# Kernel optimization log

Hardware: AMD Instinct MI355X
Metric: run time of the kernel (lower is better)

The kernel has to match this reference:

```python
import jax, jax.numpy as jnp
import numpy as np


def setup_inputs() -> dict:
    key = jax.random.key(0)
    k1, k2, k3 = jax.random.split(key, 3)
    B, H, W = 32, 512, 512
    N = H * W  # tokens
    K = 32768  # positive_trials
    decision_scores = jax.random.normal(k1, (B, N, 2), dtype=jnp.float32)
    s_map = jax.random.uniform(k2, (B, 1, H, W), dtype=jnp.float32)
    # uniform noise for gumbel sampling, kept away from {0,1} for log stability
    u = jax.random.uniform(k3, (B, N, 2), dtype=jnp.float32, minval=1e-6, maxval=1.0 - 1e-6)
    return {"decision_scores": decision_scores, "s_map": s_map, "u": u, "positive_trials": K}


def reference(decision_scores, s_map, u, positive_trials):
    B, N, _ = decision_scores.shape
    # gumbel_softmax(hard=False, tau=1): softmax(logits + gumbel_noise)
    gumbel = -jnp.log(-jnp.log(u))
    logp = jax.nn.log_softmax(decision_scores + gumbel, axis=-1)  # [B, N, 2]
    # soft_decisions = p[..., 0]
    # Tokenizer: [B, 1, H, W] -> [B, N, 1]; use channel 0 as salience score.
    scores = s_map.reshape(B, 1, -1).transpose(0, 2, 1)[..., 0]  # [B, N]
    # argsort descending, take top-k indices == lax.top_k indices
    _, idx = jax.lax.top_k(scores, positive_trials)  # [B, K]
    trials = jnp.zeros((B, N), dtype=decision_scores.dtype)
    trials = trials.at[jnp.arange(B)[:, None], idx].set(1.0)  # scatter ones
    # BCE(sum): -sum(t*log(p) + (1-t)*log(1-p)); with 2-class softmax, 1-p0 = p1.
    # torch BCE clamps log terms at -100.
    logp0 = jnp.clip(logp[..., 0], -100.0)
    logp1 = jnp.clip(logp[..., 1], -100.0)
    loss = -jnp.sum(trials * logp0 + (1.0 - trials) * logp1)
    return loss
```

## Files before the change

### kernel.cpp

```cpp
#include <hip/hip_runtime.h>

#define NB    4096
#define CAP   1024
#define BATCH 32
#define NTOK  262144
#define PT    1024
#define LOSS_BLOCKS 4096

__device__ __forceinline__ int bucket_of(float v) {
    int b = (int)(v * (float)NB);
    return b > NB - 1 ? NB - 1 : b;
}

__global__ __launch_bounds__(PT) void prep_kernel(const float* __restrict__ smap,
                                                  const int* __restrict__ kptr,
                                                  float* __restrict__ T,
                                                  int* __restrict__ ncut) {
    __shared__ int   hist[NB];
    __shared__ int   sA[PT];
    __shared__ int   sB[PT];
    __shared__ float sv[CAP];
    __shared__ int   si[CAP];
    __shared__ int   cnt_s, tb_s, R_s;

    const int tid = threadIdx.x;
    const int b   = blockIdx.x;

    for (int i = tid; i < NB; i += PT) hist[i] = 0;
    if (tid == 0) cnt_s = 0;
    __syncthreads();

    const float4* src = (const float4*)(smap + (size_t)b * NTOK);
    const int NF4 = NTOK / 4;
    for (int i = tid; i < NF4; i += PT) {
        float4 v = src[i];
        atomicAdd(&hist[bucket_of(v.x)], 1);
        atomicAdd(&hist[bucket_of(v.y)], 1);
        atomicAdd(&hist[bucket_of(v.z)], 1);
        atomicAdd(&hist[bucket_of(v.w)], 1);
    }
    __syncthreads();

    const int C = NB / PT;
    int base = tid * C;
    int csum = hist[base] + hist[base + 1] + hist[base + 2] + hist[base + 3];
    sA[tid] = csum;
    __syncthreads();

    int* pin = sA; int* pout = sB;
    for (int st = 1; st < PT; st <<= 1) {
        int v = pin[tid] + ((tid + st < PT) ? pin[tid + st] : 0);
        pout[tid] = v;
        __syncthreads();
        int* t_ = pin; pin = pout; pout = t_;
    }
    int above = (tid < PT - 1) ? pin[tid + 1] : 0;

    const int K = *kptr;
    int cum = above;
    for (int i = C - 1; i >= 0; i--) {
        int hb = hist[base + i];
        if (cum < K && cum + hb >= K) { tb_s = base + i; R_s = K - cum; }
        cum += hb;
    }
    __syncthreads();
    const int tb = tb_s, R = R_s;

    for (int i = tid; i < NF4; i += PT) {
        float4 v = src[i];
        float vals[4] = {v.x, v.y, v.z, v.w};
#pragma unroll
        for (int c = 0; c < 4; c++) {
            if (bucket_of(vals[c]) == tb) {
                int p = atomicAdd(&cnt_s, 1);
                if (p < CAP) { sv[p] = vals[c]; si[p] = 4 * i + c; }
            }
        }
    }
    __syncthreads();

    int M = cnt_s;
    if (M > CAP || R > M || R < 1) {
        if (tid == 0) { T[b] = (float)tb / (float)NB; ncut[b] = 0x7fffffff; }
        return;
    }
    for (int i = tid; i < M; i += PT) {
        float vi = sv[i]; int ii = si[i];
        int r = 0;
        for (int j = 0; j < M; j++) {
            float vj = sv[j];
            r += (vj > vi) || (vj == vi && si[j] < ii);
        }
        if (r == R - 1) { T[b] = vi; ncut[b] = ii; }
    }
}

__device__ __forceinline__ float token_loss(float d0, float d1, float u0, float u1,
                                            bool sel) {
    float g0 = -__logf(-__logf(u0));
    float g1 = -__logf(-__logf(u1));
    float dd = (d0 + g0) - (d1 + g1);
    float l  = __logf(1.f + __expf(-fabsf(dd)));
    float lp0 = (dd >= 0.f) ? -l      : dd - l;
    float lp1 = (dd >= 0.f) ? -l - dd : -l;
    lp0 = fmaxf(lp0, -100.f); lp1 = fmaxf(lp1, -100.f);
    return sel ? -lp0 : -lp1;
}

__global__ void loss_kernel(const float* __restrict__ ds, const float* __restrict__ u,
                            const float* __restrict__ smap, const float* __restrict__ T,
                            const int* __restrict__ ncut, float* __restrict__ partials) {
    int tid = blockIdx.x * blockDim.x + threadIdx.x;
    int b  = tid >> 15;
    int p8 = tid & 32767;
    const float4* ds4 = (const float4*)(ds + (size_t)b * NTOK * 2);
    const float4* u4  = (const float4*)(u  + (size_t)b * NTOK * 2);
    const float4* s4  = (const float4*)(smap + (size_t)b * NTOK);

    float4 d0 = ds4[4 * p8 + 0];
    float4 d1 = ds4[4 * p8 + 1];
    float4 d2 = ds4[4 * p8 + 2];
    float4 d3 = ds4[4 * p8 + 3];
    float4 u0 = u4[4 * p8 + 0];
    float4 u1 = u4[4 * p8 + 1];
    float4 u2 = u4[4 * p8 + 2];
    float4 u3 = u4[4 * p8 + 3];
    float4 sa = s4[2 * p8 + 0];
    float4 sb = s4[2 * p8 + 1];

    float Tb = T[b];
    int   nc = ncut[b];
    int   n0 = p8 << 3;

    bool e0 = (sa.x > Tb) || (sa.x == Tb && (n0 + 0) <= nc);
    bool e1 = (sa.y > Tb) || (sa.y == Tb && (n0 + 1) <= nc);
    bool e2 = (sa.z > Tb) || (sa.z == Tb && (n0 + 2) <= nc);
    bool e3 = (sa.w > Tb) || (sa.w == Tb && (n0 + 3) <= nc);
    bool e4 = (sb.x > Tb) || (sb.x == Tb && (n0 + 4) <= nc);
    bool e5 = (sb.y > Tb) || (sb.y == Tb && (n0 + 5) <= nc);
    bool e6 = (sb.z > Tb) || (sb.z == Tb && (n0 + 6) <= nc);
    bool e7 = (sb.w > Tb) || (sb.w == Tb && (n0 + 7) <= nc);

    float acc = token_loss(d0.x, d0.y, u0.x, u0.y, e0)
              + token_loss(d0.z, d0.w, u0.z, u0.w, e1)
              + token_loss(d1.x, d1.y, u1.x, u1.y, e2)
              + token_loss(d1.z, d1.w, u1.z, u1.w, e3)
              + token_loss(d2.x, d2.y, u2.x, u2.y, e4)
              + token_loss(d2.z, d2.w, u2.z, u2.w, e5)
              + token_loss(d3.x, d3.y, u3.x, u3.y, e6)
              + token_loss(d3.z, d3.w, u3.z, u3.w, e7);

    for (int off = 32; off > 0; off >>= 1) acc += __shfl_down(acc, off, 64);
    __shared__ float red[4];
    int lane = threadIdx.x & 63, wv = threadIdx.x >> 6;
    if (lane == 0) red[wv] = acc;
    __syncthreads();
    if (threadIdx.x == 0)
        partials[blockIdx.x] = red[0] + red[1] + red[2] + red[3];
}

__global__ void reduce_kernel(const float* __restrict__ partials, float* __restrict__ out) {
    float acc = 0.f;
    for (int i = threadIdx.x; i < LOSS_BLOCKS; i += blockDim.x) acc += partials[i];
    for (int off = 32; off > 0; off >>= 1) acc += __shfl_down(acc, off, 64);
    __shared__ float red[16];
    int lane = threadIdx.x & 63, wv = threadIdx.x >> 6;
    if (lane == 0) red[wv] = acc;
    __syncthreads();
    if (threadIdx.x == 0) {
        float s = 0.f;
        for (int w = 0; w < (int)(blockDim.x >> 6); w++) s += red[w];
        out[0] = s;
    }
}

extern "C" void kernel_launch(void* const* d_in, const int* in_sizes, int n_in,
                              void* d_out, int out_size, void* d_ws, size_t ws_size,
                              hipStream_t stream) {
    const float* ds   = (const float*)d_in[0];
    const float* smap = (const float*)d_in[1];
    const float* u    = (const float*)d_in[2];
    const int*   kptr = (const int*)d_in[3];

    float* T    = (float*)d_ws;
    int*   ncut = (int*)(T + BATCH);
    float* partials = (float*)(ncut + BATCH);

    prep_kernel<<<BATCH, PT, 0, stream>>>(smap, kptr, T, ncut);
    loss_kernel<<<LOSS_BLOCKS, 256, 0, stream>>>(ds, u, smap, T, ncut, partials);
    reduce_kernel<<<1, 1024, 0, stream>>>(partials, (float*)d_out);
}
```

Before: 233.9 us.

## Split top-k threshold prep into multi-block histogram, select, collect and refine kernels

The single prep kernel ran only one block per batch (32 blocks) and streamed each batch's salience map twice. It is replaced by a 512-block histogram kernel writing partial histograms to global memory, a select kernel that merges them and finds the threshold bucket, a 256-block collect kernel that gathers candidates with global atomics, and a refine kernel that ranks them. The loss kernel also switches to nontemporal loads for the decision scores and noise. The aim is to spread the salience scan across many more CUs, at the cost of extra launches, global histogram traffic and global atomic contention.

```diff
diff --git a/kernel.cpp b/kernel.cpp
--- a/kernel.cpp
+++ b/kernel.cpp
@@ -4,87 +4,128 @@
 #define CAP   1024
 #define BATCH 32
 #define NTOK  262144
-#define PT    1024
+#define HB    512
+#define HPB   16
 #define LOSS_BLOCKS 4096
+
+typedef float floatx4 __attribute__((ext_vector_type(4)));
 
 __device__ __forceinline__ int bucket_of(float v) {
     int b = (int)(v * (float)NB);
     return b > NB - 1 ? NB - 1 : b;
 }
 
-__global__ __launch_bounds__(PT) void prep_kernel(const float* __restrict__ smap,
-                                                  const int* __restrict__ kptr,
-                                                  float* __restrict__ T,
-                                                  int* __restrict__ ncut) {
-    __shared__ int   hist[NB];
-    __shared__ int   sA[PT];
-    __shared__ int   sB[PT];
-    __shared__ float sv[CAP];
-    __shared__ int   si[CAP];
-    __shared__ int   cnt_s, tb_s, R_s;
-
+__global__ void hist_kernel(const float* __restrict__ smap, int* __restrict__ ghist) {
+    __shared__ int lh[NB];
+    for (int i = threadIdx.x; i < NB; i += 256) lh[i] = 0;
+    __syncthreads();
+    const int b  = blockIdx.x / HPB;
+    const int cb = blockIdx.x % HPB;
+    const int chunk = NTOK / HPB;
+    const float4* src = (const float4*)(smap + (size_t)b * NTOK + (size_t)cb * chunk);
+    for (int i = threadIdx.x; i < chunk / 4; i += 256) {
+        float4 v = src[i];
+        atomicAdd(&lh[bucket_of(v.x)], 1);
+        atomicAdd(&lh[bucket_of(v.y)], 1);
+        atomicAdd(&lh[bucket_of(v.z)], 1);
+        atomicAdd(&lh[bucket_of(v.w)], 1);
+    }
+    __syncthreads();
+    int* out = ghist + (size_t)blockIdx.x * NB;
+    for (int i = threadIdx.x; i < NB; i += 256) out[i] = lh[i];
+}
+
+__global__ __launch_bounds__(1024) void select_kernel(const int* __restrict__ ghist,
+                                                      const int* __restrict__ kptr,
+                                                      int* __restrict__ tbR,
+                                                      int* __restrict__ cnt) {
+    __shared__ int hist[NB];
+    __shared__ int sA[1024];
+    __shared__ int sB[1024];
     const int tid = threadIdx.x;
     const int b   = blockIdx.x;
-
-    for (int i = tid; i < NB; i += PT) hist[i] = 0;
-    if (tid == 0) cnt_s = 0;
-    __syncthreads();
-
-    const float4* src = (const float4*)(smap + (size_t)b * NTOK);
-    const int NF4 = NTOK / 4;
-    for (int i = tid; i < NF4; i += PT) {
-        float4 v = src[i];
-        atomicAdd(&hist[bucket_of(v.x)], 1);
-        atomicAdd(&hist[bucket_of(v.y)], 1);
-        atomicAdd(&hist[bucket_of(v.z)], 1);
-        atomicAdd(&hist[bucket_of(v.w)], 1);
-    }
-    __syncthreads();
-
-    const int C = NB / PT;
+    if (tid == 0) cnt[b] = 0;
+
+    const int C = NB / 1024;
     int base = tid * C;
+    const int* gh0 = ghist + (size_t)b * HPB * NB;
+#pragma unroll
+    for (int i = 0; i < C; i++) {
+        int s = 0;
+        for (int c = 0; c < HPB; c++) s += gh0[c * NB + base + i];
+        hist[base + i] = s;
+    }
     int csum = hist[base] + hist[base + 1] + hist[base + 2] + hist[base + 3];
     sA[tid] = csum;
     __syncthreads();
 
     int* pin = sA; int* pout = sB;
-    for (int st = 1; st < PT; st <<= 1) {
-        int v = pin[tid] + ((tid + st < PT) ? pin[tid + st] : 0);
+    for (int st = 1; st < 1024; st <<= 1) {
+        int v = pin[tid] + ((tid + st < 1024) ? pin[tid + st] : 0);
         pout[tid] = v;
         __syncthreads();
         int* t_ = pin; pin = pout; pout = t_;
     }
-    int above = (tid < PT - 1) ? pin[tid + 1] : 0;
+    int above = (tid < 1023) ? pin[tid + 1] : 0;
 
     const int K = *kptr;
     int cum = above;
     for (int i = C - 1; i >= 0; i--) {
         int hb = hist[base + i];
-        if (cum < K && cum + hb >= K) { tb_s = base + i; R_s = K - cum; }
+        if (cum < K && cum + hb >= K) {
+            tbR[2 * b]     = base + i;
+            tbR[2 * b + 1] = K - cum;
+        }
         cum += hb;
     }
-    __syncthreads();
-    const int tb = tb_s, R = R_s;
-
-    for (int i = tid; i < NF4; i += PT) {
+}
+
+__global__ void collect_kernel(const float* __restrict__ smap, const int* __restrict__ tbR,
+                               int* __restrict__ cnt, float* __restrict__ cval,
+                               int* __restrict__ cidx) {
+    const int cbpb = 8;
+    const int b  = blockIdx.x / cbpb;
+    const int cb = blockIdx.x % cbpb;
+    const int chunk = NTOK / cbpb;
+    const int tb = tbR[2 * b];
+    const float4* src = (const float4*)(smap + (size_t)b * NTOK + (size_t)cb * chunk);
+    const int base_n = cb * chunk;
+    for (int i = threadIdx.x; i < chunk / 4; i += 256) {
         float4 v = src[i];
         float vals[4] = {v.x, v.y, v.z, v.w};
 #pragma unroll
-        for (int c = 0; c < 4; c++) {
-            if (bucket_of(vals[c]) == tb) {
-                int p = atomicAdd(&cnt_s, 1);
-                if (p < CAP) { sv[p] = vals[c]; si[p] = 4 * i + c; }
+        for (int s = 0; s < 4; s++) {
+            if (bucket_of(vals[s]) == tb) {
+                int p = atomicAdd(&cnt[b], 1);
+                if (p < CAP) {
+                    cval[b * CAP + p] = vals[s];
+                    cidx[b * CAP + p] = base_n + 4 * i + s;
+                }
             }
         }
     }
-    __syncthreads();
-
-    int M = cnt_s;
-    if (M > CAP || R > M || R < 1) {
-        if (tid == 0) { T[b] = (float)tb / (float)NB; ncut[b] = 0x7fffffff; }
+}
+
+__global__ void refine_kernel(const int* __restrict__ tbR, const int* __restrict__ cnt,
+                              const float* __restrict__ cval, const int* __restrict__ cidx,
+                              float* __restrict__ T, int* __restrict__ ncut) {
+    const int b = blockIdx.x;
+    const int R = tbR[2 * b + 1];
+    int M = cnt[b];
+    bool ovf = (M > CAP);
+    if (M > CAP) M = CAP;
+    __shared__ float sv[CAP];
+    __shared__ int   si[CAP];
+    for (int i = threadIdx.x; i < M; i += 256) {
+        sv[i] = cval[b * CAP + i];
+        si[i] = cidx[b * CAP + i];
+    }
+    __syncthreads();
+    if (ovf || R > M || R < 1) {
+        if (threadIdx.x == 0) { T[b] = (float)tbR[2 * b] / (float)NB; ncut[b] = 0x7fffffff; }
         return;
     }
-    for (int i = tid; i < M; i += PT) {
+    for (int i = threadIdx.x; i < M; i += 256) {
         float vi = sv[i]; int ii = si[i];
         int r = 0;
         for (int j = 0; j < M; j++) {
@@ -113,18 +154,18 @@
     int tid = blockIdx.x * blockDim.x + threadIdx.x;
     int b  = tid >> 15;
     int p8 = tid & 32767;
-    const float4* ds4 = (const float4*)(ds + (size_t)b * NTOK * 2);
-    const float4* u4  = (const float4*)(u  + (size_t)b * NTOK * 2);
-    const float4* s4  = (const float4*)(smap + (size_t)b * NTOK);
-
-    float4 d0 = ds4[4 * p8 + 0];
-    float4 d1 = ds4[4 * p8 + 1];
-    float4 d2 = ds4[4 * p8 + 2];
-    float4 d3 = ds4[4 * p8 + 3];
-    float4 u0 = u4[4 * p8 + 0];
-    float4 u1 = u4[4 * p8 + 1];
-    float4 u2 = u4[4 * p8 + 2];
-    float4 u3 = u4[4 * p8 + 3];
+    const floatx4* ds4 = (const floatx4*)(ds + (size_t)b * NTOK * 2);
+    const floatx4* u4  = (const floatx4*)(u  + (size_t)b * NTOK * 2);
+    const float4*  s4  = (const float4*)(smap + (size_t)b * NTOK);
+
+    floatx4 d0 = __builtin_nontemporal_load(&ds4[4 * p8 + 0]);
+    floatx4 d1 = __builtin_nontemporal_load(&ds4[4 * p8 + 1]);
+    floatx4 d2 = __builtin_nontemporal_load(&ds4[4 * p8 + 2]);
+    floatx4 d3 = __builtin_nontemporal_load(&ds4[4 * p8 + 3]);
+    floatx4 u0 = __builtin_nontemporal_load(&u4[4 * p8 + 0]);
+    floatx4 u1 = __builtin_nontemporal_load(&u4[4 * p8 + 1]);
+    floatx4 u2 = __builtin_nontemporal_load(&u4[4 * p8 + 2]);
+    floatx4 u3 = __builtin_nontemporal_load(&u4[4 * p8 + 3]);
     float4 sa = s4[2 * p8 + 0];
     float4 sb = s4[2 * p8 + 1];
 
@@ -182,11 +223,19 @@
     const float* u    = (const float*)d_in[2];
     const int*   kptr = (const int*)d_in[3];
 
-    float* T    = (float*)d_ws;
-    int*   ncut = (int*)(T + BATCH);
-    float* partials = (float*)(ncut + BATCH);
-
-    prep_kernel<<<BATCH, PT, 0, stream>>>(smap, kptr, T, ncut);
+    int*   ghist = (int*)d_ws;
+    int*   cnt   = ghist + HB * NB;
+    int*   tbR   = cnt + BATCH;
+    float* T     = (float*)(tbR + 2 * BATCH);
+    int*   ncut  = (int*)(T + BATCH);
+    float* cval  = (float*)(ncut + BATCH);
+    int*   cidx  = (int*)(cval + BATCH * CAP);
+    float* partials = (float*)(cidx + BATCH * CAP);
+
+    hist_kernel<<<HB, 256, 0, stream>>>(smap, ghist);
+    select_kernel<<<BATCH, 1024, 0, stream>>>(ghist, kptr, tbR, cnt);
+    collect_kernel<<<256, 256, 0, stream>>>(smap, tbR, cnt, cval, cidx);
+    refine_kernel<<<BATCH, 256, 0, stream>>>(tbR, cnt, cval, cidx, T, ncut);
     loss_kernel<<<LOSS_BLOCKS, 256, 0, stream>>>(ds, u, smap, T, ncut, partials);
     reduce_kernel<<<1, 1024, 0, stream>>>(partials, (float*)d_out);
 }
```

After: 213.1 us. -8.9%, faster.
